# Performance work log

Measured on AMD Instinct MI355X. Metric: run time of the kernel, lower is better.

## Reference

```python
import jax, jax.numpy as jnp
import numpy as np

K = 16  # knn


def conv1x1(x, w, b):
    # x: (B,Cin,k,N), w: (Cout,Cin), b: (Cout,)
    return jnp.einsum('oc,bckn->bokn', w, x) + b[None, :, None, None]


def leaky(x):
    return jnp.where(x >= 0, x, 0.2 * x)


def conv_res(x, sc_w, sc_b, a_w, a_b, b_w, b_b, c_w, c_b):
    sc = conv1x1(x, sc_w, sc_b)
    h = leaky(conv1x1(x, a_w, a_b))
    h = leaky(conv1x1(h, b_w, b_b))
    h = conv1x1(h, c_w, c_b)
    return h + sc


def get_knn_feature(xyz, k):
    # xyz: (B,3,N) -> feature (B,10,k,N)
    x_t = jnp.transpose(xyz, (0, 2, 1))  # (B,N,3)
    xx = jnp.sum(x_t * x_t, axis=-1)  # (B,N)
    inner = jnp.einsum('bnc,bmc->bnm', x_t, x_t)  # (B,N,N)
    d2 = xx[:, :, None] + xx[:, None, :] - 2.0 * inner  # squared dists
    _, idx = jax.lax.top_k(-d2, k)  # (B,N,k) nearest (includes self)
    neighbors = jax.vmap(lambda pts, i: pts[i])(x_t, idx)  # (B,N,k,3)
    center = x_t[:, :, None, :]  # (B,N,1,3)
    rel = neighbors - center
    dist = jnp.sqrt(jnp.sum(rel * rel, axis=-1, keepdims=True) + 1e-12)  # (B,N,k,1)
    feat = jnp.concatenate([jnp.broadcast_to(center, neighbors.shape), neighbors, rel, dist], axis=-1)  # (B,N,k,10)
    return jnp.transpose(feat, (0, 3, 2, 1))  # (B,10,k,N)


def _mk_w(key, o, i):
    s = 1.0 / np.sqrt(i)
    return jax.random.uniform(key, (o, i), jnp.float32, -s, s)


def setup_inputs():
    key = jax.random.key(0)
    ks = jax.random.split(key, 20)
    B, N = 4, 8192
    hide, out = 64, 128
    inp = {'xyz': jax.random.normal(ks[0], (B, 3, N), jnp.float32)}
    # CONV_Res(10, 64, 64)
    inp['p1_sc_w'] = _mk_w(ks[1], hide, 10); inp['p1_sc_b'] = jnp.zeros((hide,), jnp.float32)
    inp['p1_a_w'] = _mk_w(ks[2], hide, 10); inp['p1_a_b'] = jnp.zeros((hide,), jnp.float32)
    inp['p1_b_w'] = _mk_w(ks[3], hide, hide); inp['p1_b_b'] = jnp.zeros((hide,), jnp.float32)
    inp['p1_c_w'] = _mk_w(ks[4], hide, hide); inp['p1_c_b'] = jnp.zeros((hide,), jnp.float32)
    # CONV_Res(128, 64, 128)
    inp['p2_sc_w'] = _mk_w(ks[5], out, 2 * hide); inp['p2_sc_b'] = jnp.zeros((out,), jnp.float32)
    inp['p2_a_w'] = _mk_w(ks[6], hide, 2 * hide); inp['p2_a_b'] = jnp.zeros((hide,), jnp.float32)
    inp['p2_b_w'] = _mk_w(ks[7], out, hide); inp['p2_b_b'] = jnp.zeros((out,), jnp.float32)
    inp['p2_c_w'] = _mk_w(ks[8], out, out); inp['p2_c_b'] = jnp.zeros((out,), jnp.float32)
    return inp


def reference(xyz, p1_sc_w, p1_sc_b, p1_a_w, p1_a_b, p1_b_w, p1_b_b, p1_c_w, p1_c_b,
              p2_sc_w, p2_sc_b, p2_a_w, p2_a_b, p2_b_w, p2_b_b, p2_c_w, p2_c_b):
    x = get_knn_feature(xyz, K)  # (B,10,k,N)
    x = conv_res(x, p1_sc_w, p1_sc_b, p1_a_w, p1_a_b, p1_b_w, p1_b_b, p1_c_w, p1_c_b)  # (B,64,k,N)
    x1 = jnp.max(x, axis=2, keepdims=True)  # (B,64,1,N)
    x1 = jnp.broadcast_to(x1, x.shape)  # repeat over k
    x = jnp.concatenate([x, x1], axis=1)  # (B,128,k,N)
    x = conv_res(x, p2_sc_w, p2_sc_b, p2_a_w, p2_a_b, p2_b_w, p2_b_b, p2_c_w, p2_c_b)  # (B,128,k,N)
    return jnp.max(x, axis=2)  # (B,128,N)
```

## Files before the change

kernel.cpp:

```cpp
#include <hip/hip_runtime.h>
#include <hip/hip_bf16.h>

#define B_ 4
#define N_ 8192
#define KNN 16
#define BN_ (B_*N_)
#define NPOS (BN_*KNN)

typedef __attribute__((ext_vector_type(8))) short bf16x8;
typedef __attribute__((ext_vector_type(4))) float f32x4;

static __device__ __forceinline__ unsigned short f2bf(float f) {
  union { float f; unsigned u; } v; v.f = f;
  unsigned r = v.u + 0x7fff + ((v.u >> 16) & 1);
  return (unsigned short)(r >> 16);
}
static __device__ __forceinline__ float lk(float x) { return x >= 0.f ? x : 0.2f*x; }
static __device__ __forceinline__ unsigned pk2(float a, float b) {
  return (unsigned)f2bf(a) | ((unsigned)f2bf(b) << 16);
}

__global__ void k_prep(const float* __restrict__ xyz, float4* __restrict__ pts4) {
  int i = blockIdx.x * 256 + threadIdx.x;
  if (i >= BN_) return;
  int b = i >> 13, n = i & (N_-1);
  const float* p = xyz + b*3*N_;
  float x = p[n], y = p[N_+n], z = p[2*N_+n];
  float xx = fmaf(z, z, fmaf(y, y, x*x));
  pts4[i] = make_float4(x, y, z, xx);
}

__global__ void k_wcvt(const float* __restrict__ w_sc, const float* __restrict__ w_a,
                       const float* __restrict__ w_b, const float* __restrict__ w_c,
                       unsigned short* __restrict__ out) {
  int i = blockIdx.x*256 + threadIdx.x;
  if (i >= 49152) return;
  int x = i*2;
  const float* w; int base, K2;
  if (x < 32768)      { w = w_sc; base = 0;     K2 = 256; }
  else if (x < 49152) { w = w_a;  base = 32768; K2 = 256; }
  else if (x < 65536) { w = w_b;  base = 49152; K2 = 128; }
  else                { w = w_c;  base = 65536; K2 = 256; }
  int off = x - base;
  int row = off / K2;
  int colb = (off & (K2-1)) ^ ((row & 7) << 4);
  int k = colb >> 1;
  out[i] = f2bf(w[row*(K2 >> 1) + k]);
}

__global__ __launch_bounds__(512) void k_knn(const float4* __restrict__ pts4,
                                             int* __restrict__ knn) {
  __shared__ float4 cand[2048];
  const int lane = threadIdx.x & 63;
  const int wv   = threadIdx.x >> 6;
  const int q = blockIdx.x * 8 + wv;
  const int b = q >> 13;
  const int n = q & (N_-1);
  const float4* __restrict__ P = pts4 + (b << 13);
  float4 me = P[n];

  float av = __builtin_inff(); int ai = 0;
  float worst = __builtin_inff();

  for (int ch = 0; ch < 4; ++ch) {
    __syncthreads();
    #pragma unroll
    for (int t = 0; t < 4; ++t)
      cand[t*512 + threadIdx.x] = P[ch*2048 + t*512 + threadIdx.x];
    __syncthreads();

    int it0 = 0;
    if (ch == 0) {
      float4 c = cand[lane];
      float dot = fmaf(me.z, c.z, fmaf(me.y, c.y, me.x*c.x));
      float v = (me.w + c.w) - 2.0f*dot;
      int id = lane;
      #pragma unroll
      for (int size = 2; size <= 64; size <<= 1) {
        #pragma unroll
        for (int stride = size >> 1; stride >= 1; stride >>= 1) {
          float ov = __shfl_xor(v, stride);
          int   oi = __shfl_xor(id, stride);
          bool up = ((lane & size) == 0);
          bool keepmin = (((lane & stride) == 0) == up);
          bool oless = (ov < v) || (ov == v && oi < id);
          if (oless == keepmin) { v = ov; id = oi; }
        }
      }
      av = (lane < 16) ? v : __builtin_inff();
      ai = id;
      worst = __shfl(av, 15);
      it0 = 1;
    }

    for (int it = it0; it < 32; ++it) {
      int ci = it*64 + lane;
      float4 c = cand[ci];
      float dot = fmaf(me.z, c.z, fmaf(me.y, c.y, me.x*c.x));
      float d2 = (me.w + c.w) - 2.0f*dot;
      int cid = ch*2048 + ci;
      unsigned long long m = __ballot(d2 < worst);
      if (m) {
        do {
          int src = __ffsll(m) - 1;
          m &= (m - 1);
          float v = __shfl(d2, src);
          int  id = __shfl(cid, src);
          int p = __popcll(__ballot((lane < 16) && (av <= v)));
          if (p < 16) {
            float pav = __shfl_up(av, 1);
            int   pai = __shfl_up(ai, 1);
            if (lane >= p) { av = (lane == p) ? v : pav; ai = (lane == p) ? id : pai; }
          }
        } while (m);
        worst = __shfl(av, 15);
      }
    }
  }
  if (lane < 16) knn[(q << 4) + lane] = ai;
}

__global__ __launch_bounds__(512, 4) void k_p1(
    const float4* __restrict__ pts4, const int* __restrict__ knn,
    const float* __restrict__ a_w, const float* __restrict__ a_b,
    const float* __restrict__ b_w, const float* __restrict__ b_b,
    const float* __restrict__ c_w, const float* __restrict__ c_b,
    const float* __restrict__ sc_w, const float* __restrict__ sc_b,
    unsigned short* __restrict__ X, unsigned short* __restrict__ XM) {
  __shared__ __align__(16) unsigned short Ws1[12288];
  __shared__ __align__(16) unsigned short Fs[8192];
  __shared__ __align__(16) unsigned short Hr[16384];
  const int tid = threadIdx.x;
  const int lane = tid & 63, wv = tid >> 6;
  const int colr = lane & 15, kq = lane >> 4;
  const int bn0 = blockIdx.x * 16;

  if (tid < 256) {
    int bnl = tid >> 4, kk = tid & 15;
    int bn = bn0 + bnl;
    int b = bn >> 13;
    float4 cp = pts4[bn];
    int nid = knn[bn*16 + kk];
    float4 np = pts4[(b << 13) + nid];
    float rx = np.x - cp.x, ry = np.y - cp.y, rz = np.z - cp.z;
    float dist = sqrtf(fmaf(rz, rz, fmaf(ry, ry, rx*rx)) + 1e-12f);
    unsigned short row[32];
    row[0]=f2bf(cp.x); row[1]=f2bf(cp.y); row[2]=f2bf(cp.z);
    row[3]=f2bf(np.x); row[4]=f2bf(np.y); row[5]=f2bf(np.z);
    row[6]=f2bf(rx);   row[7]=f2bf(ry);   row[8]=f2bf(rz);   row[9]=f2bf(dist);
    #pragma unroll
    for (int j = 10; j < 32; ++j) row[j] = 0;
    int wvp = tid >> 5, posl = tid & 31;
    char* dst = (char*)Fs + wvp*2048 + posl*64;
    #pragma unroll
    for (int c = 0; c < 4; ++c)
      *(uint4*)(dst + ((c*16) ^ ((posl&3)<<4))) = *(const uint4*)(row + c*8);
  } else {
    int tt = tid - 256;
    for (int i = 0; i < 48; ++i) {
      int e = i*256 + tt;
      float val; int byteoff;
      if (e < 2048) {
        int row = e >> 5, k = e & 31;
        val = (k < 10) ? a_w[row*10 + k] : 0.f;
        byteoff = row*64 + ((2*k) ^ ((row&3)<<4));
      } else if (e < 4096) {
        int le = e - 2048, row = le >> 5, k = le & 31;
        val = (k < 10) ? sc_w[row*10 + k] : 0.f;
        byteoff = 4096 + row*64 + ((2*k) ^ ((row&3)<<4));
      } else if (e < 8192) {
        int le = e - 4096, row = le >> 6, k = le & 63;
        val = b_w[row*64 + k];
        byteoff = 8192 + row*128 + ((2*k) ^ ((row&7)<<4));
      } else {
        int le = e - 8192, row = le >> 6, k = le & 63;
        val = c_w[row*64 + k];
        byteoff = 16384 + row*128 + ((2*k) ^ ((row&7)<<4));
      }
      *(unsigned short*)((char*)Ws1 + byteoff) = f2bf(val);
    }
  }
  __syncthreads();

  const char* WS = (const char*)Ws1;

  bf16x8 bf[2];
  #pragma unroll
  for (int ct = 0; ct < 2; ++ct) {
    int posl = ct*16 + colr;
    bf[ct] = *(const bf16x8*)((const char*)Fs + wv*2048 + posl*64 + ((kq*16) ^ ((posl&3)<<4)));
  }

  f32x4 acc[4][2];
  #pragma unroll
  for (int mt = 0; mt < 4; ++mt) {
    int r0 = mt*16 + kq*4;
    #pragma unroll
    for (int r = 0; r < 4; ++r) {
      float bia = c_b[r0+r] + sc_b[r0+r];
      acc[mt][0][r] = bia; acc[mt][1][r] = bia;
    }
  }
  #pragma unroll
  for (int mt = 0; mt < 4; ++mt) {
    int row = mt*16 + colr;
    bf16x8 w = *(const bf16x8*)(WS + 4096 + row*64 + ((kq*16) ^ ((row&3)<<4)));
    acc[mt][0] = __builtin_amdgcn_mfma_f32_16x16x32_bf16(w, bf[0], acc[mt][0], 0, 0, 0);
    acc[mt][1] = __builtin_amdgcn_mfma_f32_16x16x32_bf16(w, bf[1], acc[mt][1], 0, 0, 0);
  }

  f32x4 ha[4][2];
  #pragma unroll
  for (int mt = 0; mt < 4; ++mt) {
    int r0 = mt*16 + kq*4;
    #pragma unroll
    for (int r = 0; r < 4; ++r) { ha[mt][0][r] = a_b[r0+r]; ha[mt][1][r] = a_b[r0+r]; }
  }
  #pragma unroll
  for (int mt = 0; mt < 4; ++mt) {
    int row = mt*16 + colr;
    bf16x8 w = *(const bf16x8*)(WS + row*64 + ((kq*16) ^ ((row&3)<<4)));
    ha[mt][0] = __builtin_amdgcn_mfma_f32_16x16x32_bf16(w, bf[0], ha[mt][0], 0, 0, 0);
    ha[mt][1] = __builtin_amdgcn_mfma_f32_16x16x32_bf16(w, bf[1], ha[mt][1], 0, 0, 0);
  }

  char* H = (char*)Hr + wv*4096;
  #pragma unroll
  for (int mt = 0; mt < 4; ++mt) {
    int ch2 = (mt*16 + kq*4) * 2;
    #pragma unroll
    for (int ct = 0; ct < 2; ++ct) {
      int posl = ct*16 + colr;
      uint2 u;
      u.x = pk2(lk(ha[mt][ct][0]), lk(ha[mt][ct][1]));
      u.y = pk2(lk(ha[mt][ct][2]), lk(ha[mt][ct][3]));
      *(uint2*)(H + posl*128 + (ch2 ^ ((posl&7)<<4))) = u;
    }
  }
  bf16x8 bh[2][2];
  #pragma unroll
  for (int ct = 0; ct < 2; ++ct) {
    int posl = ct*16 + colr;
    #pragma unroll
    for (int k2 = 0; k2 < 2; ++k2)
      bh[ct][k2] = *(const bf16x8*)(H + posl*128 + ((k2*64 + kq*16) ^ ((posl&7)<<4)));
  }

  #pragma unroll
  for (int jj = 0; jj < 2; ++jj) {
    f32x4 h2[2][2];
    #pragma unroll
    for (int mtp = 0; mtp < 2; ++mtp) {
      int r0 = (jj*2 + mtp)*16 + kq*4;
      #pragma unroll
      for (int r = 0; r < 4; ++r) { h2[mtp][0][r] = b_b[r0+r]; h2[mtp][1][r] = b_b[r0+r]; }
    }
    #pragma unroll
    for (int mtp = 0; mtp < 2; ++mtp) {
      int row = (jj*2 + mtp)*16 + colr;
      #pragma unroll
      for (int k2 = 0; k2 < 2; ++k2) {
        bf16x8 w = *(const bf16x8*)(WS + 8192 + row*128 + ((k2*64 + kq*16) ^ ((row&7)<<4)));
        h2[mtp][0] = __builtin_amdgcn_mfma_f32_16x16x32_bf16(w, bh[0][k2], h2[mtp][0], 0, 0, 0);
        h2[mtp][1] = __builtin_amdgcn_mfma_f32_16x16x32_bf16(w, bh[1][k2], h2[mtp][1], 0, 0, 0);
      }
    }
    #pragma unroll
    for (int mtp = 0; mtp < 2; ++mtp) {
      int ch2 = ((jj*2 + mtp)*16 + kq*4) * 2;
      #pragma unroll
      for (int ct = 0; ct < 2; ++ct) {
        int posl = ct*16 + colr;
        uint2 u;
        u.x = pk2(lk(h2[mtp][ct][0]), lk(h2[mtp][ct][1]));
        u.y = pk2(lk(h2[mtp][ct][2]), lk(h2[mtp][ct][3]));
        *(uint2*)(H + posl*128 + (ch2 ^ ((posl&7)<<4))) = u;
      }
    }
    bf16x8 b2[2];
    #pragma unroll
    for (int ct = 0; ct < 2; ++ct) {
      int posl = ct*16 + colr;
      b2[ct] = *(const bf16x8*)(H + posl*128 + ((jj*64 + kq*16) ^ ((posl&7)<<4)));
    }
    #pragma unroll
    for (int mt = 0; mt < 4; ++mt) {
      int row = mt*16 + colr;
      bf16x8 w = *(const bf16x8*)(WS + 16384 + row*128 + ((jj*64 + kq*16) ^ ((row&7)<<4)));
      acc[mt][0] = __builtin_amdgcn_mfma_f32_16x16x32_bf16(w, b2[0], acc[mt][0], 0, 0, 0);
      acc[mt][1] = __builtin_amdgcn_mfma_f32_16x16x32_bf16(w, b2[1], acc[mt][1], 0, 0, 0);
    }
  }

  #pragma unroll
  for (int ct = 0; ct < 2; ++ct) {
    int bn = bn0 + wv*2 + ct;
    #pragma unroll
    for (int mt = 0; mt < 4; ++mt) {
      int ch0 = mt*16 + kq*4;
      uint2 u;
      u.x = pk2(acc[mt][ct][0], acc[mt][ct][1]);
      u.y = pk2(acc[mt][ct][2], acc[mt][ct][3]);
      *(uint2*)(X + ((size_t)(bn*16 + colr))*64 + ch0) = u;
      float m[4];
      #pragma unroll
      for (int r = 0; r < 4; ++r) {
        float v = acc[mt][ct][r];
        v = fmaxf(v, __shfl_xor(v, 1));
        v = fmaxf(v, __shfl_xor(v, 2));
        v = fmaxf(v, __shfl_xor(v, 4));
        v = fmaxf(v, __shfl_xor(v, 8));
        m[r] = v;
      }
      if (colr == 0) {
        uint2 um; um.x = pk2(m[0], m[1]); um.y = pk2(m[2], m[3]);
        *(uint2*)(XM + (size_t)bn*64 + ch0) = um;
      }
    }
  }
}

__global__ __launch_bounds__(512, 2) void k_p2(
    const unsigned short* __restrict__ X, const unsigned short* __restrict__ XM,
    const unsigned short* __restrict__ wbf,
    const float* __restrict__ sc_b, const float* __restrict__ a_b,
    const float* __restrict__ b_b, const float* __restrict__ c_b,
    float* __restrict__ out) {
  __shared__ __align__(16) unsigned short Ws[49152];
  __shared__ __align__(16) unsigned short Hr[8][2048];
  __shared__ __align__(16) float outT[128][16];
  const int tid = threadIdx.x;
  const int lane = tid & 63, wv = tid >> 6;
  const int colr = lane & 15, kq = lane >> 4;
  const int bn0 = blockIdx.x * 16;

  bf16x8 bx[2][4];
  #pragma unroll
  for (int ct = 0; ct < 2; ++ct) {
    int bn = bn0 + wv*2 + ct;
    const unsigned short* xr = X + ((size_t)bn*16 + colr)*64 + kq*8;
    bx[ct][0] = *(const bf16x8*)(xr);
    bx[ct][1] = *(const bf16x8*)(xr + 32);
    const unsigned short* mr = XM + (size_t)bn*64 + kq*8;
    bx[ct][2] = *(const bf16x8*)(mr);
    bx[ct][3] = *(const bf16x8*)(mr + 32);
  }

  for (int it = 0; it < 12; ++it) {
    int c = it*512 + tid;
    *(uint4*)((char*)Ws + c*16) = *(const uint4*)((const char*)wbf + c*16);
  }
  __syncthreads();

  const char* WSC = (const char*)Ws;
  const char* WA  = (const char*)(Ws + 16384);
  const char* WB  = (const char*)(Ws + 24576);
  const char* WC  = (const char*)(Ws + 32768);

#define WF(base, row, K2, ksbyte) \
  (*(const bf16x8*)((base) + (row)*(K2) + ((((ksbyte) + kq*16)) ^ (((row)&7)<<4))))

  f32x4 acc[8][2];
  #pragma unroll
  for (int mt = 0; mt < 8; ++mt) {
    int r0 = mt*16 + kq*4;
    #pragma unroll
    for (int r = 0; r < 4; ++r) {
      float bia = c_b[r0+r] + sc_b[r0+r];
      acc[mt][0][r] = bia; acc[mt][1][r] = bia;
    }
  }
  #pragma unroll
  for (int mt = 0; mt < 8; ++mt) {
    int row = mt*16 + colr;
    #pragma unroll
    for (int ks = 0; ks < 4; ++ks) {
      bf16x8 w = WF(WSC, row, 256, ks*64);
      acc[mt][0] = __builtin_amdgcn_mfma_f32_16x16x32_bf16(w, bx[0][ks], acc[mt][0], 0, 0, 0);
      acc[mt][1] = __builtin_amdgcn_mfma_f32_16x16x32_bf16(w, bx[1][ks], acc[mt][1], 0, 0, 0);
    }
  }

  f32x4 ha[4][2];
  #pragma unroll
  for (int mt = 0; mt < 4; ++mt) {
    int r0 = mt*16 + kq*4;
    #pragma unroll
    for (int r = 0; r < 4; ++r) { ha[mt][0][r] = a_b[r0+r]; ha[mt][1][r] = a_b[r0+r]; }
  }
  #pragma unroll
  for (int mt = 0; mt < 4; ++mt) {
    int row = mt*16 + colr;
    #pragma unroll
    for (int ks = 0; ks < 4; ++ks) {
      bf16x8 w = WF(WA, row, 256, ks*64);
      ha[mt][0] = __builtin_amdgcn_mfma_f32_16x16x32_bf16(w, bx[0][ks], ha[mt][0], 0, 0, 0);
      ha[mt][1] = __builtin_amdgcn_mfma_f32_16x16x32_bf16(w, bx[1][ks], ha[mt][1], 0, 0, 0);
    }
  }

  char* H = (char*)Hr[wv];
  #pragma unroll
  for (int mt = 0; mt < 4; ++mt) {
    int ch2 = (mt*16 + kq*4) * 2;
    #pragma unroll
    for (int ct = 0; ct < 2; ++ct) {
      int posl = ct*16 + colr;
      uint2 u;
      u.x = pk2(lk(ha[mt][ct][0]), lk(ha[mt][ct][1]));
      u.y = pk2(lk(ha[mt][ct][2]), lk(ha[mt][ct][3]));
      *(uint2*)(H + posl*128 + (ch2 ^ ((posl&7)<<4))) = u;
    }
  }
  bf16x8 bh[2][2];
  #pragma unroll
  for (int ct = 0; ct < 2; ++ct) {
    int posl = ct*16 + colr;
    #pragma unroll
    for (int k2 = 0; k2 < 2; ++k2)
      bh[ct][k2] = *(const bf16x8*)(H + posl*128 + ((k2*64 + kq*16) ^ ((posl&7)<<4)));
  }

  #pragma unroll
  for (int j = 0; j < 4; ++j) {
    f32x4 h2[2][2];
    #pragma unroll
    for (int mtp = 0; mtp < 2; ++mtp) {
      int r0 = (2*j + mtp)*16 + kq*4;
      #pragma unroll
      for (int r = 0; r < 4; ++r) { h2[mtp][0][r] = b_b[r0+r]; h2[mtp][1][r] = b_b[r0+r]; }
    }
    #pragma unroll
    for (int mtp = 0; mtp < 2; ++mtp) {
      int row = (2*j + mtp)*16 + colr;
      #pragma unroll
      for (int k2 = 0; k2 < 2; ++k2) {
        bf16x8 w = WF(WB, row, 128, k2*64);
        h2[mtp][0] = __builtin_amdgcn_mfma_f32_16x16x32_bf16(w, bh[0][k2], h2[mtp][0], 0, 0, 0);
        h2[mtp][1] = __builtin_amdgcn_mfma_f32_16x16x32_bf16(w, bh[1][k2], h2[mtp][1], 0, 0, 0);
      }
    }
    char* PB = H + (j & 1)*2048;
    #pragma unroll
    for (int mtp = 0; mtp < 2; ++mtp) {
      int chp2 = (mtp*16 + kq*4) * 2;
      #pragma unroll
      for (int ct = 0; ct < 2; ++ct) {
        int posl = ct*16 + colr;
        uint2 u;
        u.x = pk2(lk(h2[mtp][ct][0]), lk(h2[mtp][ct][1]));
        u.y = pk2(lk(h2[mtp][ct][2]), lk(h2[mtp][ct][3]));
        *(uint2*)(PB + posl*64 + (chp2 ^ ((posl&3)<<4))) = u;
      }
    }
    bf16x8 b2[2];
    #pragma unroll
    for (int ct = 0; ct < 2; ++ct) {
      int posl = ct*16 + colr;
      b2[ct] = *(const bf16x8*)(PB + posl*64 + ((kq*16) ^ ((posl&3)<<4)));
    }
    #pragma unroll
    for (int mt = 0; mt < 8; ++mt) {
      int row = mt*16 + colr;
      bf16x8 w = WF(WC, row, 256, j*64);
      acc[mt][0] = __builtin_amdgcn_mfma_f32_16x16x32_bf16(w, b2[0], acc[mt][0], 0, 0, 0);
      acc[mt][1] = __builtin_amdgcn_mfma_f32_16x16x32_bf16(w, b2[1], acc[mt][1], 0, 0, 0);
    }
  }
#undef WF

  #pragma unroll
  for (int mt = 0; mt < 8; ++mt) {
    #pragma unroll
    for (int ct = 0; ct < 2; ++ct) {
      #pragma unroll
      for (int r = 0; r < 4; ++r) {
        float v = acc[mt][ct][r];
        v = fmaxf(v, __shfl_xor(v, 1));
        v = fmaxf(v, __shfl_xor(v, 2));
        v = fmaxf(v, __shfl_xor(v, 4));
        v = fmaxf(v, __shfl_xor(v, 8));
        if (colr == 0) outT[mt*16 + kq*4 + r][wv*2 + ct] = v;
      }
    }
  }
  __syncthreads();
  {
    int ch = tid >> 2, p = tid & 3;
    int b = bn0 >> 13, n0 = bn0 & (N_-1);
    float4 v4 = *(const float4*)&outT[ch][p*4];
    *(float4*)(out + ((size_t)b*128 + ch)*N_ + n0 + p*4) = v4;
  }
}

extern "C" void kernel_launch(void* const* d_in, const int* in_sizes, int n_in,
                              void* d_out, int out_size, void* d_ws, size_t ws_size,
                              hipStream_t stream) {
  const float* xyz     = (const float*)d_in[0];
  const float* p1_sc_w = (const float*)d_in[1];
  const float* p1_sc_b = (const float*)d_in[2];
  const float* p1_a_w  = (const float*)d_in[3];
  const float* p1_a_b  = (const float*)d_in[4];
  const float* p1_b_w  = (const float*)d_in[5];
  const float* p1_b_b  = (const float*)d_in[6];
  const float* p1_c_w  = (const float*)d_in[7];
  const float* p1_c_b  = (const float*)d_in[8];
  const float* p2_sc_w = (const float*)d_in[9];
  const float* p2_sc_b = (const float*)d_in[10];
  const float* p2_a_w  = (const float*)d_in[11];
  const float* p2_a_b  = (const float*)d_in[12];
  const float* p2_b_w  = (const float*)d_in[13];
  const float* p2_b_b  = (const float*)d_in[14];
  const float* p2_c_w  = (const float*)d_in[15];
  const float* p2_c_b  = (const float*)d_in[16];

  if (ws_size < 75497472u) return;
  char* ws = (char*)d_ws;
  float4* pts4        = (float4*)(ws);
  unsigned short* wbf = (unsigned short*)(ws + 524288);
  int* knn            = (int*)(ws + 655360);
  unsigned short* X   = (unsigned short*)(ws + 4194304);
  unsigned short* XM  = (unsigned short*)(ws + 4194304 + 67108864);
  float* out = (float*)d_out;

  k_prep<<<dim3(BN_/256), dim3(256), 0, stream>>>(xyz, pts4);
  k_wcvt<<<dim3(192), dim3(256), 0, stream>>>(p2_sc_w, p2_a_w, p2_b_w, p2_c_w, wbf);
  k_knn<<<dim3(BN_/8), dim3(512), 0, stream>>>(pts4, knn);
  k_p1<<<dim3(NPOS/256), dim3(512), 0, stream>>>(pts4, knn,
      p1_a_w, p1_a_b, p1_b_w, p1_b_b, p1_c_w, p1_c_b, p1_sc_w, p1_sc_b, X, XM);
  k_p2<<<dim3(NPOS/256), dim3(512), 0, stream>>>(X, XM, wbf,
      p2_sc_b, p2_a_b, p2_b_b, p2_c_b, out);
}
```

Measured before the change: 429.7 us.

## Persist p1/p2 blocks over multiple tiles and preconvert p1 weights once

Stage-1 weights are now converted to swizzled bf16 once in the weight-conversion kernel, so k_p1 only copies them into shared memory. Both MLP kernels are made persistent over several point tiles (4 in p1, 8 in p2), so each block loads its weights into LDS once and reuses them across tiles. k_p2 also prefetches the next tile's input fragments into registers while the current tile computes. The cost is fewer blocks and less parallelism, extra registers for the prefetch buffers, and added barriers per tile.

```diff
diff --git a/kernel.cpp b/kernel.cpp
--- a/kernel.cpp
+++ b/kernel.cpp
@@ -32,20 +32,45 @@
 
 __global__ void k_wcvt(const float* __restrict__ w_sc, const float* __restrict__ w_a,
                        const float* __restrict__ w_b, const float* __restrict__ w_c,
+                       const float* __restrict__ p1a, const float* __restrict__ p1sc,
+                       const float* __restrict__ p1b, const float* __restrict__ p1c,
                        unsigned short* __restrict__ out) {
   int i = blockIdx.x*256 + threadIdx.x;
-  if (i >= 49152) return;
-  int x = i*2;
-  const float* w; int base, K2;
-  if (x < 32768)      { w = w_sc; base = 0;     K2 = 256; }
-  else if (x < 49152) { w = w_a;  base = 32768; K2 = 256; }
-  else if (x < 65536) { w = w_b;  base = 49152; K2 = 128; }
-  else                { w = w_c;  base = 65536; K2 = 256; }
-  int off = x - base;
-  int row = off / K2;
-  int colb = (off & (K2-1)) ^ ((row & 7) << 4);
-  int k = colb >> 1;
-  out[i] = f2bf(w[row*(K2 >> 1) + k]);
+  if (i >= 61440) return;
+  if (i < 49152) {
+    int x = i*2;
+    const float* w; int base, K2;
+    if (x < 32768)      { w = w_sc; base = 0;     K2 = 256; }
+    else if (x < 49152) { w = w_a;  base = 32768; K2 = 256; }
+    else if (x < 65536) { w = w_b;  base = 49152; K2 = 128; }
+    else                { w = w_c;  base = 65536; K2 = 256; }
+    int off = x - base;
+    int row = off / K2;
+    int colb = (off & (K2-1)) ^ ((row & 7) << 4);
+    int k = colb >> 1;
+    out[i] = f2bf(w[row*(K2 >> 1) + k]);
+  } else {
+    int e = i - 49152;
+    float val; int byteoff;
+    if (e < 2048) {
+      int row = e >> 5, k = e & 31;
+      val = (k < 10) ? p1a[row*10 + k] : 0.f;
+      byteoff = row*64 + ((2*k) ^ ((row & 3) << 4));
+    } else if (e < 4096) {
+      int le = e - 2048, row = le >> 5, k = le & 31;
+      val = (k < 10) ? p1sc[row*10 + k] : 0.f;
+      byteoff = 4096 + row*64 + ((2*k) ^ ((row & 3) << 4));
+    } else if (e < 8192) {
+      int le = e - 4096, row = le >> 6, k = le & 63;
+      val = p1b[row*64 + k];
+      byteoff = 8192 + row*128 + ((2*k) ^ ((row & 7) << 4));
+    } else {
+      int le = e - 8192, row = le >> 6, k = le & 63;
+      val = p1c[row*64 + k];
+      byteoff = 16384 + row*128 + ((2*k) ^ ((row & 7) << 4));
+    }
+    out[49152 + (byteoff >> 1)] = f2bf(val);
+  }
 }
 
 __global__ __launch_bounds__(512) void k_knn(const float4* __restrict__ pts4,
@@ -122,10 +147,9 @@
 
 __global__ __launch_bounds__(512, 4) void k_p1(
     const float4* __restrict__ pts4, const int* __restrict__ knn,
-    const float* __restrict__ a_w, const float* __restrict__ a_b,
-    const float* __restrict__ b_w, const float* __restrict__ b_b,
-    const float* __restrict__ c_w, const float* __restrict__ c_b,
-    const float* __restrict__ sc_w, const float* __restrict__ sc_b,
+    const unsigned short* __restrict__ wbf,
+    const float* __restrict__ a_b, const float* __restrict__ b_b,
+    const float* __restrict__ c_b, const float* __restrict__ sc_b,
     unsigned short* __restrict__ X, unsigned short* __restrict__ XM) {
   __shared__ __align__(16) unsigned short Ws1[12288];
   __shared__ __align__(16) unsigned short Fs[8192];
@@ -133,190 +157,195 @@
   const int tid = threadIdx.x;
   const int lane = tid & 63, wv = tid >> 6;
   const int colr = lane & 15, kq = lane >> 4;
-  const int bn0 = blockIdx.x * 16;
-
-  if (tid < 256) {
-    int bnl = tid >> 4, kk = tid & 15;
-    int bn = bn0 + bnl;
-    int b = bn >> 13;
-    float4 cp = pts4[bn];
-    int nid = knn[bn*16 + kk];
-    float4 np = pts4[(b << 13) + nid];
-    float rx = np.x - cp.x, ry = np.y - cp.y, rz = np.z - cp.z;
-    float dist = sqrtf(fmaf(rz, rz, fmaf(ry, ry, rx*rx)) + 1e-12f);
-    unsigned short row[32];
-    row[0]=f2bf(cp.x); row[1]=f2bf(cp.y); row[2]=f2bf(cp.z);
-    row[3]=f2bf(np.x); row[4]=f2bf(np.y); row[5]=f2bf(np.z);
-    row[6]=f2bf(rx);   row[7]=f2bf(ry);   row[8]=f2bf(rz);   row[9]=f2bf(dist);
-    #pragma unroll
-    for (int j = 10; j < 32; ++j) row[j] = 0;
-    int wvp = tid >> 5, posl = tid & 31;
-    char* dst = (char*)Fs + wvp*2048 + posl*64;
-    #pragma unroll
-    for (int c = 0; c < 4; ++c)
-      *(uint4*)(dst + ((c*16) ^ ((posl&3)<<4))) = *(const uint4*)(row + c*8);
-  } else {
-    int tt = tid - 256;
-    for (int i = 0; i < 48; ++i) {
-      int e = i*256 + tt;
-      float val; int byteoff;
-      if (e < 2048) {
-        int row = e >> 5, k = e & 31;
-        val = (k < 10) ? a_w[row*10 + k] : 0.f;
-        byteoff = row*64 + ((2*k) ^ ((row&3)<<4));
-      } else if (e < 4096) {
-        int le = e - 2048, row = le >> 5, k = le & 31;
-        val = (k < 10) ? sc_w[row*10 + k] : 0.f;
-        byteoff = 4096 + row*64 + ((2*k) ^ ((row&3)<<4));
-      } else if (e < 8192) {
-        int le = e - 4096, row = le >> 6, k = le & 63;
-        val = b_w[row*64 + k];
-        byteoff = 8192 + row*128 + ((2*k) ^ ((row&7)<<4));
-      } else {
-        int le = e - 8192, row = le >> 6, k = le & 63;
-        val = c_w[row*64 + k];
-        byteoff = 16384 + row*128 + ((2*k) ^ ((row&7)<<4));
-      }
-      *(unsigned short*)((char*)Ws1 + byteoff) = f2bf(val);
-    }
-  }
-  __syncthreads();
-
+
+  #pragma unroll
+  for (int j = 0; j < 3; ++j) {
+    int c = j*512 + tid;
+    ((uint4*)Ws1)[c] = ((const uint4*)(wbf + 49152))[c];
+  }
   const char* WS = (const char*)Ws1;
-
-  bf16x8 bf[2];
-  #pragma unroll
-  for (int ct = 0; ct < 2; ++ct) {
-    int posl = ct*16 + colr;
-    bf[ct] = *(const bf16x8*)((const char*)Fs + wv*2048 + posl*64 + ((kq*16) ^ ((posl&3)<<4)));
-  }
-
-  f32x4 acc[4][2];
-  #pragma unroll
-  for (int mt = 0; mt < 4; ++mt) {
-    int r0 = mt*16 + kq*4;
-    #pragma unroll
-    for (int r = 0; r < 4; ++r) {
-      float bia = c_b[r0+r] + sc_b[r0+r];
-      acc[mt][0][r] = bia; acc[mt][1][r] = bia;
-    }
-  }
-  #pragma unroll
-  for (int mt = 0; mt < 4; ++mt) {
-    int row = mt*16 + colr;
-    bf16x8 w = *(const bf16x8*)(WS + 4096 + row*64 + ((kq*16) ^ ((row&3)<<4)));
-    acc[mt][0] = __builtin_amdgcn_mfma_f32_16x16x32_bf16(w, bf[0], acc[mt][0], 0, 0, 0);
-    acc[mt][1] = __builtin_amdgcn_mfma_f32_16x16x32_bf16(w, bf[1], acc[mt][1], 0, 0, 0);
-  }
-
-  f32x4 ha[4][2];
-  #pragma unroll
-  for (int mt = 0; mt < 4; ++mt) {
-    int r0 = mt*16 + kq*4;
-    #pragma unroll
-    for (int r = 0; r < 4; ++r) { ha[mt][0][r] = a_b[r0+r]; ha[mt][1][r] = a_b[r0+r]; }
-  }
-  #pragma unroll
-  for (int mt = 0; mt < 4; ++mt) {
-    int row = mt*16 + colr;
-    bf16x8 w = *(const bf16x8*)(WS + row*64 + ((kq*16) ^ ((row&3)<<4)));
-    ha[mt][0] = __builtin_amdgcn_mfma_f32_16x16x32_bf16(w, bf[0], ha[mt][0], 0, 0, 0);
-    ha[mt][1] = __builtin_amdgcn_mfma_f32_16x16x32_bf16(w, bf[1], ha[mt][1], 0, 0, 0);
-  }
-
   char* H = (char*)Hr + wv*4096;
-  #pragma unroll
-  for (int mt = 0; mt < 4; ++mt) {
-    int ch2 = (mt*16 + kq*4) * 2;
+
+  for (int tile = 0; tile < 4; ++tile) {
+    const int bn0 = (blockIdx.x*4 + tile) * 16;
+    __syncthreads();
+    if (tid < 256) {
+      int bnl = tid >> 4, kk = tid & 15;
+      int bn = bn0 + bnl;
+      int b = bn >> 13;
+      float4 cp = pts4[bn];
+      int nid = knn[bn*16 + kk];
+      float4 np = pts4[(b << 13) + nid];
+      float rx = np.x - cp.x, ry = np.y - cp.y, rz = np.z - cp.z;
+      float dist = sqrtf(fmaf(rz, rz, fmaf(ry, ry, rx*rx)) + 1e-12f);
+      unsigned short row[32];
+      row[0]=f2bf(cp.x); row[1]=f2bf(cp.y); row[2]=f2bf(cp.z);
+      row[3]=f2bf(np.x); row[4]=f2bf(np.y); row[5]=f2bf(np.z);
+      row[6]=f2bf(rx);   row[7]=f2bf(ry);   row[8]=f2bf(rz);   row[9]=f2bf(dist);
+      #pragma unroll
+      for (int j = 10; j < 32; ++j) row[j] = 0;
+      int wvp = tid >> 5, posl = tid & 31;
+      char* dst = (char*)Fs + wvp*2048 + posl*64;
+      #pragma unroll
+      for (int c = 0; c < 4; ++c)
+        *(uint4*)(dst + ((c*16) ^ ((posl&3)<<4))) = *(const uint4*)(row + c*8);
+    }
+    __syncthreads();
+
+    bf16x8 bfr[2];
     #pragma unroll
     for (int ct = 0; ct < 2; ++ct) {
       int posl = ct*16 + colr;
-      uint2 u;
-      u.x = pk2(lk(ha[mt][ct][0]), lk(ha[mt][ct][1]));
-      u.y = pk2(lk(ha[mt][ct][2]), lk(ha[mt][ct][3]));
-      *(uint2*)(H + posl*128 + (ch2 ^ ((posl&7)<<4))) = u;
-    }
-  }
-  bf16x8 bh[2][2];
-  #pragma unroll
-  for (int ct = 0; ct < 2; ++ct) {
-    int posl = ct*16 + colr;
-    #pragma unroll
-    for (int k2 = 0; k2 < 2; ++k2)
-      bh[ct][k2] = *(const bf16x8*)(H + posl*128 + ((k2*64 + kq*16) ^ ((posl&7)<<4)));
-  }
-
-  #pragma unroll
-  for (int jj = 0; jj < 2; ++jj) {
-    f32x4 h2[2][2];
-    #pragma unroll
-    for (int mtp = 0; mtp < 2; ++mtp) {
-      int r0 = (jj*2 + mtp)*16 + kq*4;
-      #pragma unroll
-      for (int r = 0; r < 4; ++r) { h2[mtp][0][r] = b_b[r0+r]; h2[mtp][1][r] = b_b[r0+r]; }
-    }
-    #pragma unroll
-    for (int mtp = 0; mtp < 2; ++mtp) {
-      int row = (jj*2 + mtp)*16 + colr;
-      #pragma unroll
-      for (int k2 = 0; k2 < 2; ++k2) {
-        bf16x8 w = *(const bf16x8*)(WS + 8192 + row*128 + ((k2*64 + kq*16) ^ ((row&7)<<4)));
-        h2[mtp][0] = __builtin_amdgcn_mfma_f32_16x16x32_bf16(w, bh[0][k2], h2[mtp][0], 0, 0, 0);
-        h2[mtp][1] = __builtin_amdgcn_mfma_f32_16x16x32_bf16(w, bh[1][k2], h2[mtp][1], 0, 0, 0);
-      }
-    }
-    #pragma unroll
-    for (int mtp = 0; mtp < 2; ++mtp) {
-      int ch2 = ((jj*2 + mtp)*16 + kq*4) * 2;
+      bfr[ct] = *(const bf16x8*)((const char*)Fs + wv*2048 + posl*64 + ((kq*16) ^ ((posl&3)<<4)));
+    }
+
+    f32x4 acc[4][2];
+    #pragma unroll
+    for (int mt = 0; mt < 4; ++mt) {
+      int r0 = mt*16 + kq*4;
+      #pragma unroll
+      for (int r = 0; r < 4; ++r) {
+        float bia = c_b[r0+r] + sc_b[r0+r];
+        acc[mt][0][r] = bia; acc[mt][1][r] = bia;
+      }
+    }
+    #pragma unroll
+    for (int mt = 0; mt < 4; ++mt) {
+      int row = mt*16 + colr;
+      bf16x8 w = *(const bf16x8*)(WS + 4096 + row*64 + ((kq*16) ^ ((row&3)<<4)));
+      acc[mt][0] = __builtin_amdgcn_mfma_f32_16x16x32_bf16(w, bfr[0], acc[mt][0], 0, 0, 0);
+      acc[mt][1] = __builtin_amdgcn_mfma_f32_16x16x32_bf16(w, bfr[1], acc[mt][1], 0, 0, 0);
+    }
+
+    f32x4 ha[4][2];
+    #pragma unroll
+    for (int mt = 0; mt < 4; ++mt) {
+      int r0 = mt*16 + kq*4;
+      #pragma unroll
+      for (int r = 0; r < 4; ++r) { ha[mt][0][r] = a_b[r0+r]; ha[mt][1][r] = a_b[r0+r]; }
+    }
+    #pragma unroll
+    for (int mt = 0; mt < 4; ++mt) {
+      int row = mt*16 + colr;
+      bf16x8 w = *(const bf16x8*)(WS + row*64 + ((kq*16) ^ ((row&3)<<4)));
+      ha[mt][0] = __builtin_amdgcn_mfma_f32_16x16x32_bf16(w, bfr[0], ha[mt][0], 0, 0, 0);
+      ha[mt][1] = __builtin_amdgcn_mfma_f32_16x16x32_bf16(w, bfr[1], ha[mt][1], 0, 0, 0);
+    }
+
+    #pragma unroll
+    for (int mt = 0; mt < 4; ++mt) {
+      int ch2 = (mt*16 + kq*4) * 2;
       #pragma unroll
       for (int ct = 0; ct < 2; ++ct) {
         int posl = ct*16 + colr;
         uint2 u;
-        u.x = pk2(lk(h2[mtp][ct][0]), lk(h2[mtp][ct][1]));
-        u.y = pk2(lk(h2[mtp][ct][2]), lk(h2[mtp][ct][3]));
+        u.x = pk2(lk(ha[mt][ct][0]), lk(ha[mt][ct][1]));
+        u.y = pk2(lk(ha[mt][ct][2]), lk(ha[mt][ct][3]));
         *(uint2*)(H + posl*128 + (ch2 ^ ((posl&7)<<4))) = u;
       }
     }
-    bf16x8 b2[2];
+    bf16x8 bh[2][2];
     #pragma unroll
     for (int ct = 0; ct < 2; ++ct) {
       int posl = ct*16 + colr;
-      b2[ct] = *(const bf16x8*)(H + posl*128 + ((jj*64 + kq*16) ^ ((posl&7)<<4)));
-    }
-    #pragma unroll
-    for (int mt = 0; mt < 4; ++mt) {
-      int row = mt*16 + colr;
-      bf16x8 w = *(const bf16x8*)(WS + 16384 + row*128 + ((jj*64 + kq*16) ^ ((row&7)<<4)));
-      acc[mt][0] = __builtin_amdgcn_mfma_f32_16x16x32_bf16(w, b2[0], acc[mt][0], 0, 0, 0);
-      acc[mt][1] = __builtin_amdgcn_mfma_f32_16x16x32_bf16(w, b2[1], acc[mt][1], 0, 0, 0);
-    }
-  }
-
+      #pragma unroll
+      for (int k2 = 0; k2 < 2; ++k2)
+        bh[ct][k2] = *(const bf16x8*)(H + posl*128 + ((k2*64 + kq*16) ^ ((posl&7)<<4)));
+    }
+
+    #pragma unroll
+    for (int jj = 0; jj < 2; ++jj) {
+      f32x4 h2[2][2];
+      #pragma unroll
+      for (int mtp = 0; mtp < 2; ++mtp) {
+        int r0 = (jj*2 + mtp)*16 + kq*4;
+        #pragma unroll
+        for (int r = 0; r < 4; ++r) { h2[mtp][0][r] = b_b[r0+r]; h2[mtp][1][r] = b_b[r0+r]; }
+      }
+      #pragma unroll
+      for (int mtp = 0; mtp < 2; ++mtp) {
+        int row = (jj*2 + mtp)*16 + colr;
+        #pragma unroll
+        for (int k2 = 0; k2 < 2; ++k2) {
+          bf16x8 w = *(const bf16x8*)(WS + 8192 + row*128 + ((k2*64 + kq*16) ^ ((row&7)<<4)));
+          h2[mtp][0] = __builtin_amdgcn_mfma_f32_16x16x32_bf16(w, bh[0][k2], h2[mtp][0], 0, 0, 0);
+          h2[mtp][1] = __builtin_amdgcn_mfma_f32_16x16x32_bf16(w, bh[1][k2], h2[mtp][1], 0, 0, 0);
+        }
+      }
+      #pragma unroll
+      for (int mtp = 0; mtp < 2; ++mtp) {
+        int ch2 = ((jj*2 + mtp)*16 + kq*4) * 2;
+        #pragma unroll
+        for (int ct = 0; ct < 2; ++ct) {
+          int posl = ct*16 + colr;
+          uint2 u;
+          u.x = pk2(lk(h2[mtp][ct][0]), lk(h2[mtp][ct][1]));
+          u.y = pk2(lk(h2[mtp][ct][2]), lk(h2[mtp][ct][3]));
+          *(uint2*)(H + posl*128 + (ch2 ^ ((posl&7)<<4))) = u;
+        }
+      }
+      bf16x8 b2[2];
+      #pragma unroll
+      for (int ct = 0; ct < 2; ++ct) {
+        int posl = ct*16 + colr;
+        b2[ct] = *(const bf16x8*)(H + posl*128 + ((jj*64 + kq*16) ^ ((posl&7)<<4)));
+      }
+      #pragma unroll
+      for (int mt = 0; mt < 4; ++mt) {
+        int row = mt*16 + colr;
+        bf16x8 w = *(const bf16x8*)(WS + 16384 + row*128 + ((jj*64 + kq*16) ^ ((row&7)<<4)));
+        acc[mt][0] = __builtin_amdgcn_mfma_f32_16x16x32_bf16(w, b2[0], acc[mt][0], 0, 0, 0);
+        acc[mt][1] = __builtin_amdgcn_mfma_f32_16x16x32_bf16(w, b2[1], acc[mt][1], 0, 0, 0);
+      }
+    }
+
+    #pragma unroll
+    for (int ct = 0; ct < 2; ++ct) {
+      int bn = bn0 + wv*2 + ct;
+      #pragma unroll
+      for (int mt = 0; mt < 4; ++mt) {
+        int ch0 = mt*16 + kq*4;
+        uint2 u;
+        u.x = pk2(acc[mt][ct][0], acc[mt][ct][1]);
+        u.y = pk2(acc[mt][ct][2], acc[mt][ct][3]);
+        *(uint2*)(X + ((size_t)(bn*16 + colr))*64 + ch0) = u;
+        float m[4];
+        #pragma unroll
+        for (int r = 0; r < 4; ++r) {
+          float v = acc[mt][ct][r];
+          v = fmaxf(v, __shfl_xor(v, 1));
+          v = fmaxf(v, __shfl_xor(v, 2));
+          v = fmaxf(v, __shfl_xor(v, 4));
+          v = fmaxf(v, __shfl_xor(v, 8));
+          m[r] = v;
+        }
+        if (colr == 0) {
+          uint2 um; um.x = pk2(m[0], m[1]); um.y = pk2(m[2], m[3]);
+          *(uint2*)(XM + (size_t)bn*64 + ch0) = um;
+        }
+      }
+    }
+  }
+}
+
+struct P2Shared {
+  unsigned short Ws[49152];
+  unsigned short Hr[8][2048];
+  float outT[128][16];
+};
+
+static __device__ __forceinline__ void p2_loadbx(
+    bf16x8 (&dst)[2][4], const unsigned short* __restrict__ X,
+    const unsigned short* __restrict__ XM, int bn0, int wv, int colr, int kq) {
   #pragma unroll
   for (int ct = 0; ct < 2; ++ct) {
     int bn = bn0 + wv*2 + ct;
-    #pragma unroll
-    for (int mt = 0; mt < 4; ++mt) {
-      int ch0 = mt*16 + kq*4;
-      uint2 u;
-      u.x = pk2(acc[mt][ct][0], acc[mt][ct][1]);
-      u.y = pk2(acc[mt][ct][2], acc[mt][ct][3]);
-      *(uint2*)(X + ((size_t)(bn*16 + colr))*64 + ch0) = u;
-      float m[4];
-      #pragma unroll
-      for (int r = 0; r < 4; ++r) {
-        float v = acc[mt][ct][r];
-        v = fmaxf(v, __shfl_xor(v, 1));
-        v = fmaxf(v, __shfl_xor(v, 2));
-        v = fmaxf(v, __shfl_xor(v, 4));
-        v = fmaxf(v, __shfl_xor(v, 8));
-        m[r] = v;
-      }
-      if (colr == 0) {
-        uint2 um; um.x = pk2(m[0], m[1]); um.y = pk2(m[2], m[3]);
-        *(uint2*)(XM + (size_t)bn*64 + ch0) = um;
-      }
-    }
+    const unsigned short* xr = X + ((size_t)bn*16 + colr)*64 + kq*8;
+    dst[ct][0] = *(const bf16x8*)(xr);
+    dst[ct][1] = *(const bf16x8*)(xr + 32);
+    const unsigned short* mr = XM + (size_t)bn*64 + kq*8;
+    dst[ct][2] = *(const bf16x8*)(mr);
+    dst[ct][3] = *(const bf16x8*)(mr + 32);
   }
 }
 
@@ -326,171 +355,176 @@
     const float* __restrict__ sc_b, const float* __restrict__ a_b,
     const float* __restrict__ b_b, const float* __restrict__ c_b,
     float* __restrict__ out) {
-  __shared__ __align__(16) unsigned short Ws[49152];
-  __shared__ __align__(16) unsigned short Hr[8][2048];
-  __shared__ __align__(16) float outT[128][16];
+  __shared__ __align__(16) P2Shared S;
   const int tid = threadIdx.x;
   const int lane = tid & 63, wv = tid >> 6;
   const int colr = lane & 15, kq = lane >> 4;
-  const int bn0 = blockIdx.x * 16;
-
-  bf16x8 bx[2][4];
+
   #pragma unroll
-  for (int ct = 0; ct < 2; ++ct) {
-    int bn = bn0 + wv*2 + ct;
-    const unsigned short* xr = X + ((size_t)bn*16 + colr)*64 + kq*8;
-    bx[ct][0] = *(const bf16x8*)(xr);
-    bx[ct][1] = *(const bf16x8*)(xr + 32);
-    const unsigned short* mr = XM + (size_t)bn*64 + kq*8;
-    bx[ct][2] = *(const bf16x8*)(mr);
-    bx[ct][3] = *(const bf16x8*)(mr + 32);
-  }
-
   for (int it = 0; it < 12; ++it) {
     int c = it*512 + tid;
-    *(uint4*)((char*)Ws + c*16) = *(const uint4*)((const char*)wbf + c*16);
-  }
-  __syncthreads();
-
-  const char* WSC = (const char*)Ws;
-  const char* WA  = (const char*)(Ws + 16384);
-  const char* WB  = (const char*)(Ws + 24576);
-  const char* WC  = (const char*)(Ws + 32768);
+    *(uint4*)((char*)S.Ws + c*16) = *(const uint4*)((const char*)wbf + c*16);
+  }
+
+  const char* WSC = (const char*)S.Ws;
+  const char* WA  = (const char*)(S.Ws + 16384);
+  const char* WB  = (const char*)(S.Ws + 24576);
+  const char* WC  = (const char*)(S.Ws + 32768);
+  char* H = (char*)S.Hr[wv];
 
 #define WF(base, row, K2, ksbyte) \
   (*(const bf16x8*)((base) + (row)*(K2) + ((((ksbyte) + kq*16)) ^ (((row)&7)<<4))))
 
-  f32x4 acc[8][2];
-  #pragma unroll
-  for (int mt = 0; mt < 8; ++mt) {
-    int r0 = mt*16 + kq*4;
-    #pragma unroll
-    for (int r = 0; r < 4; ++r) {
-      float bia = c_b[r0+r] + sc_b[r0+r];
-      acc[mt][0][r] = bia; acc[mt][1][r] = bia;
-    }
-  }
-  #pragma unroll
-  for (int mt = 0; mt < 8; ++mt) {
-    int row = mt*16 + colr;
-    #pragma unroll
-    for (int ks = 0; ks < 4; ++ks) {
-      bf16x8 w = WF(WSC, row, 256, ks*64);
-      acc[mt][0] = __builtin_amdgcn_mfma_f32_16x16x32_bf16(w, bx[0][ks], acc[mt][0], 0, 0, 0);
-      acc[mt][1] = __builtin_amdgcn_mfma_f32_16x16x32_bf16(w, bx[1][ks], acc[mt][1], 0, 0, 0);
-    }
-  }
-
-  f32x4 ha[4][2];
-  #pragma unroll
-  for (int mt = 0; mt < 4; ++mt) {
-    int r0 = mt*16 + kq*4;
-    #pragma unroll
-    for (int r = 0; r < 4; ++r) { ha[mt][0][r] = a_b[r0+r]; ha[mt][1][r] = a_b[r0+r]; }
-  }
-  #pragma unroll
-  for (int mt = 0; mt < 4; ++mt) {
-    int row = mt*16 + colr;
-    #pragma unroll
-    for (int ks = 0; ks < 4; ++ks) {
-      bf16x8 w = WF(WA, row, 256, ks*64);
-      ha[mt][0] = __builtin_amdgcn_mfma_f32_16x16x32_bf16(w, bx[0][ks], ha[mt][0], 0, 0, 0);
-      ha[mt][1] = __builtin_amdgcn_mfma_f32_16x16x32_bf16(w, bx[1][ks], ha[mt][1], 0, 0, 0);
-    }
-  }
-
-  char* H = (char*)Hr[wv];
-  #pragma unroll
-  for (int mt = 0; mt < 4; ++mt) {
-    int ch2 = (mt*16 + kq*4) * 2;
-    #pragma unroll
-    for (int ct = 0; ct < 2; ++ct) {
-      int posl = ct*16 + colr;
-      uint2 u;
-      u.x = pk2(lk(ha[mt][ct][0]), lk(ha[mt][ct][1]));
-      u.y = pk2(lk(ha[mt][ct][2]), lk(ha[mt][ct][3]));
-      *(uint2*)(H + posl*128 + (ch2 ^ ((posl&7)<<4))) = u;
-    }
-  }
-  bf16x8 bh[2][2];
-  #pragma unroll
-  for (int ct = 0; ct < 2; ++ct) {
-    int posl = ct*16 + colr;
-    #pragma unroll
-    for (int k2 = 0; k2 < 2; ++k2)
-      bh[ct][k2] = *(const bf16x8*)(H + posl*128 + ((k2*64 + kq*16) ^ ((posl&7)<<4)));
-  }
-
-  #pragma unroll
-  for (int j = 0; j < 4; ++j) {
-    f32x4 h2[2][2];
-    #pragma unroll
-    for (int mtp = 0; mtp < 2; ++mtp) {
-      int r0 = (2*j + mtp)*16 + kq*4;
-      #pragma unroll
-      for (int r = 0; r < 4; ++r) { h2[mtp][0][r] = b_b[r0+r]; h2[mtp][1][r] = b_b[r0+r]; }
-    }
-    #pragma unroll
-    for (int mtp = 0; mtp < 2; ++mtp) {
-      int row = (2*j + mtp)*16 + colr;
-      #pragma unroll
-      for (int k2 = 0; k2 < 2; ++k2) {
-        bf16x8 w = WF(WB, row, 128, k2*64);
-        h2[mtp][0] = __builtin_amdgcn_mfma_f32_16x16x32_bf16(w, bh[0][k2], h2[mtp][0], 0, 0, 0);
-        h2[mtp][1] = __builtin_amdgcn_mfma_f32_16x16x32_bf16(w, bh[1][k2], h2[mtp][1], 0, 0, 0);
-      }
-    }
-    char* PB = H + (j & 1)*2048;
-    #pragma unroll
-    for (int mtp = 0; mtp < 2; ++mtp) {
-      int chp2 = (mtp*16 + kq*4) * 2;
+  bf16x8 bx[2][4], bxn[2][4];
+  p2_loadbx(bx, X, XM, blockIdx.x*8*16, wv, colr, kq);
+  __syncthreads();
+
+  for (int t = 0; t < 8; ++t) {
+    const int bn0 = (blockIdx.x*8 + t) * 16;
+
+    f32x4 acc[8][2];
+    #pragma unroll
+    for (int mt = 0; mt < 8; ++mt) {
+      int r0 = mt*16 + kq*4;
+      #pragma unroll
+      for (int r = 0; r < 4; ++r) {
+        float bia = c_b[r0+r] + sc_b[r0+r];
+        acc[mt][0][r] = bia; acc[mt][1][r] = bia;
+      }
+    }
+    #pragma unroll
+    for (int mt = 0; mt < 8; ++mt) {
+      int row = mt*16 + colr;
+      #pragma unroll
+      for (int ks = 0; ks < 4; ++ks) {
+        bf16x8 w = WF(WSC, row, 256, ks*64);
+        acc[mt][0] = __builtin_amdgcn_mfma_f32_16x16x32_bf16(w, bx[0][ks], acc[mt][0], 0, 0, 0);
+        acc[mt][1] = __builtin_amdgcn_mfma_f32_16x16x32_bf16(w, bx[1][ks], acc[mt][1], 0, 0, 0);
+      }
+    }
+
+    f32x4 ha[4][2];
+    #pragma unroll
+    for (int mt = 0; mt < 4; ++mt) {
+      int r0 = mt*16 + kq*4;
+      #pragma unroll
+      for (int r = 0; r < 4; ++r) { ha[mt][0][r] = a_b[r0+r]; ha[mt][1][r] = a_b[r0+r]; }
+    }
+    #pragma unroll
+    for (int mt = 0; mt < 4; ++mt) {
+      int row = mt*16 + colr;
+      #pragma unroll
+      for (int ks = 0; ks < 4; ++ks) {
+        bf16x8 w = WF(WA, row, 256, ks*64);
+        ha[mt][0] = __builtin_amdgcn_mfma_f32_16x16x32_bf16(w, bx[0][ks], ha[mt][0], 0, 0, 0);
+        ha[mt][1] = __builtin_amdgcn_mfma_f32_16x16x32_bf16(w, bx[1][ks], ha[mt][1], 0, 0, 0);
+      }
+    }
+
+    {
+      int tn = (t < 7) ? (t + 1) : 7;
+      p2_loadbx(bxn, X, XM, (blockIdx.x*8 + tn) * 16, wv, colr, kq);
+    }
+
+    #pragma unroll
+    for (int mt = 0; mt < 4; ++mt) {
+      int ch2 = (mt*16 + kq*4) * 2;
       #pragma unroll
       for (int ct = 0; ct < 2; ++ct) {
         int posl = ct*16 + colr;
         uint2 u;
-        u.x = pk2(lk(h2[mtp][ct][0]), lk(h2[mtp][ct][1]));
-        u.y = pk2(lk(h2[mtp][ct][2]), lk(h2[mtp][ct][3]));
-        *(uint2*)(PB + posl*64 + (chp2 ^ ((posl&3)<<4))) = u;
-      }
-    }
-    bf16x8 b2[2];
+        u.x = pk2(lk(ha[mt][ct][0]), lk(ha[mt][ct][1]));
+        u.y = pk2(lk(ha[mt][ct][2]), lk(ha[mt][ct][3]));
+        *(uint2*)(H + posl*128 + (ch2 ^ ((posl&7)<<4))) = u;
+      }
+    }
+    bf16x8 bh[2][2];
     #pragma unroll
     for (int ct = 0; ct < 2; ++ct) {
       int posl = ct*16 + colr;
-      b2[ct] = *(const bf16x8*)(PB + posl*64 + ((kq*16) ^ ((posl&3)<<4)));
-    }
+      #pragma unroll
+      for (int k2 = 0; k2 < 2; ++k2)
+        bh[ct][k2] = *(const bf16x8*)(H + posl*128 + ((k2*64 + kq*16) ^ ((posl&7)<<4)));
+    }
+
+    #pragma unroll
+    for (int j = 0; j < 4; ++j) {
+      f32x4 h2[2][2];
+      #pragma unroll
+      for (int mtp = 0; mtp < 2; ++mtp) {
+        int r0 = (2*j + mtp)*16 + kq*4;
+        #pragma unroll
+        for (int r = 0; r < 4; ++r) { h2[mtp][0][r] = b_b[r0+r]; h2[mtp][1][r] = b_b[r0+r]; }
+      }
+      #pragma unroll
+      for (int mtp = 0; mtp < 2; ++mtp) {
+        int row = (2*j + mtp)*16 + colr;
+        #pragma unroll
+        for (int k2 = 0; k2 < 2; ++k2) {
+          bf16x8 w = WF(WB, row, 128, k2*64);
+          h2[mtp][0] = __builtin_amdgcn_mfma_f32_16x16x32_bf16(w, bh[0][k2], h2[mtp][0], 0, 0, 0);
+          h2[mtp][1] = __builtin_amdgcn_mfma_f32_16x16x32_bf16(w, bh[1][k2], h2[mtp][1], 0, 0, 0);
+        }
+      }
+      char* PB = H + (j & 1)*2048;
+      #pragma unroll
+      for (int mtp = 0; mtp < 2; ++mtp) {
+        int chp2 = (mtp*16 + kq*4) * 2;
+        #pragma unroll
+        for (int ct = 0; ct < 2; ++ct) {
+          int posl = ct*16 + colr;
+          uint2 u;
+          u.x = pk2(lk(h2[mtp][ct][0]), lk(h2[mtp][ct][1]));
+          u.y = pk2(lk(h2[mtp][ct][2]), lk(h2[mtp][ct][3]));
+          *(uint2*)(PB + posl*64 + (chp2 ^ ((posl&3)<<4))) = u;
+        }
+      }
+      bf16x8 b2[2];
+      #pragma unroll
+      for (int ct = 0; ct < 2; ++ct) {
+        int posl = ct*16 + colr;
+        b2[ct] = *(const bf16x8*)(PB + posl*64 + ((kq*16) ^ ((posl&3)<<4)));
+      }
+      #pragma unroll
+      for (int mt = 0; mt < 8; ++mt) {
+        int row = mt*16 + colr;
+        bf16x8 w = WF(WC, row, 256, j*64);
+        acc[mt][0] = __builtin_amdgcn_mfma_f32_16x16x32_bf16(w, b2[0], acc[mt][0], 0, 0, 0);
+        acc[mt][1] = __builtin_amdgcn_mfma_f32_16x16x32_bf16(w, b2[1], acc[mt][1], 0, 0, 0);
+      }
+    }
+
+    __syncthreads();
     #pragma unroll
     for (int mt = 0; mt < 8; ++mt) {
-      int row = mt*16 + colr;
-      bf16x8 w = WF(WC, row, 256, j*64);
-      acc[mt][0] = __builtin_amdgcn_mfma_f32_16x16x32_bf16(w, b2[0], acc[mt][0], 0, 0, 0);
-      acc[mt][1] = __builtin_amdgcn_mfma_f32_16x16x32_bf16(w, b2[1], acc[mt][1], 0, 0, 0);
-    }
+      #pragma unroll
+      for (int ct = 0; ct < 2; ++ct) {
+        #pragma unroll
+        for (int r = 0; r < 4; ++r) {
+          float v = acc[mt][ct][r];
+          v = fmaxf(v, __shfl_xor(v, 1));
+          v = fmaxf(v, __shfl_xor(v, 2));
+          v = fmaxf(v, __shfl_xor(v, 4));
+          v = fmaxf(v, __shfl_xor(v, 8));
+          if (colr == 0) S.outT[mt*16 + kq*4 + r][wv*2 + ct] = v;
+        }
+      }
+    }
+    __syncthreads();
+    {
+      int ch = tid >> 2, p = tid & 3;
+      int b = bn0 >> 13, n0 = bn0 & (N_-1);
+      float4 v4 = *(const float4*)&S.outT[ch][p*4];
+      *(float4*)(out + ((size_t)b*128 + ch)*N_ + n0 + p*4) = v4;
+    }
+
+    #pragma unroll
+    for (int ct = 0; ct < 2; ++ct)
+      #pragma unroll
+      for (int ks = 0; ks < 4; ++ks)
+        bx[ct][ks] = bxn[ct][ks];
   }
 #undef WF
-
-  #pragma unroll
-  for (int mt = 0; mt < 8; ++mt) {
-    #pragma unroll
-    for (int ct = 0; ct < 2; ++ct) {
-      #pragma unroll
-      for (int r = 0; r < 4; ++r) {
-        float v = acc[mt][ct][r];
-        v = fmaxf(v, __shfl_xor(v, 1));
-        v = fmaxf(v, __shfl_xor(v, 2));
-        v = fmaxf(v, __shfl_xor(v, 4));
-        v = fmaxf(v, __shfl_xor(v, 8));
-        if (colr == 0) outT[mt*16 + kq*4 + r][wv*2 + ct] = v;
-      }
-    }
-  }
-  __syncthreads();
-  {
-    int ch = tid >> 2, p = tid & 3;
-    int b = bn0 >> 13, n0 = bn0 & (N_-1);
-    float4 v4 = *(const float4*)&outT[ch][p*4];
-    *(float4*)(out + ((size_t)b*128 + ch)*N_ + n0 + p*4) = v4;
-  }
 }
 
 extern "C" void kernel_launch(void* const* d_in, const int* in_sizes, int n_in,
@@ -524,10 +558,11 @@
   float* out = (float*)d_out;
 
   k_prep<<<dim3(BN_/256), dim3(256), 0, stream>>>(xyz, pts4);
-  k_wcvt<<<dim3(192), dim3(256), 0, stream>>>(p2_sc_w, p2_a_w, p2_b_w, p2_c_w, wbf);
+  k_wcvt<<<dim3(240), dim3(256), 0, stream>>>(p2_sc_w, p2_a_w, p2_b_w, p2_c_w,
+      p1_a_w, p1_sc_w, p1_b_w, p1_c_w, wbf);
   k_knn<<<dim3(BN_/8), dim3(512), 0, stream>>>(pts4, knn);
-  k_p1<<<dim3(NPOS/256), dim3(512), 0, stream>>>(pts4, knn,
-      p1_a_w, p1_a_b, p1_b_w, p1_b_b, p1_c_w, p1_c_b, p1_sc_w, p1_sc_b, X, XM);
-  k_p2<<<dim3(NPOS/256), dim3(512), 0, stream>>>(X, XM, wbf,
+  k_p1<<<dim3(512), dim3(512), 0, stream>>>(pts4, knn, wbf,
+      p1_a_b, p1_b_b, p1_c_b, p1_sc_b, X, XM);
+  k_p2<<<dim3(256), dim3(512), 0, stream>>>(X, XM, wbf,
       p2_sc_b, p2_a_b, p2_b_b, p2_c_b, out);
 }
```

Result: faster. 404.0 us (-6.0%).
